# Kernel optimization log

Hardware: AMD Instinct MI355X
Metric: run time of the kernel (lower is better)

## Reference

```python
import jax, jax.numpy as jnp
import numpy as np

H = 256          # hidden_size
S = 4            # feature size (2D -> 4)
T_OUT = 16       # args.output // args.skip
HT_LIM = 100.0   # hardtanh limit
B = 16384
OBS = 16


def lstm_cell(x, h, c, Wih, Whh, bih, bhh):
    # PyTorch gate order: i, f, g, o
    g = x @ Wih.T + h @ Whh.T + bih + bhh  # [B, 4H]
    i, f, gg, o = jnp.split(g, 4, axis=-1)
    c = jax.nn.sigmoid(f) * c + jax.nn.sigmoid(i) * jnp.tanh(gg)
    h = jax.nn.sigmoid(o) * jnp.tanh(c)
    return h, c


def encode(seq, Wih, Whh, bih, bhh):
    # seq: [B, T, S]; single-layer LSTM, return final (h, c)
    h0 = jnp.zeros((seq.shape[0], H), seq.dtype)
    def step(carry, x):
        h, c = carry
        return lstm_cell(x, h, c, Wih, Whh, bih, bhh), None
    (h, c), _ = jax.lax.scan(step, (h0, h0), jnp.swapaxes(seq, 0, 1))
    return h, c


def setup_inputs() -> dict:
    key = jax.random.key(0)
    ks = jax.random.split(key, 32)
    sc = 0.05
    def W(k, shape):
        return (jax.random.normal(k, shape, jnp.float32) * sc)
    inp = {
        'speed': jax.random.normal(ks[0], (B, OBS, S), jnp.float32),
        'pos': jax.random.normal(ks[1], (B, OBS, S), jnp.float32),
        # speed encoder LSTM
        'sp_Wih': W(ks[2], (4 * H, S)), 'sp_Whh': W(ks[3], (4 * H, H)),
        'sp_bih': W(ks[4], (4 * H,)), 'sp_bhh': W(ks[5], (4 * H,)),
        # pos encoder LSTM
        'po_Wih': W(ks[6], (4 * H, S)), 'po_Whh': W(ks[7], (4 * H, H)),
        'po_bih': W(ks[8], (4 * H,)), 'po_bhh': W(ks[9], (4 * H,)),
        # speed decoder LSTMCell
        'dsp_Wih': W(ks[10], (4 * H, S)), 'dsp_Whh': W(ks[11], (4 * H, H)),
        'dsp_bih': W(ks[12], (4 * H,)), 'dsp_bhh': W(ks[13], (4 * H,)),
        # crossing decoder LSTMCell
        'dcr_Wih': W(ks[14], (4 * H, S)), 'dcr_Whh': W(ks[15], (4 * H, H)),
        'dcr_bih': W(ks[16], (4 * H,)), 'dcr_bhh': W(ks[17], (4 * H,)),
        # heads
        'fc_speed_W': W(ks[18], (S, H)), 'fc_speed_b': W(ks[19], (S,)),
        'fc_cross_W': W(ks[20], (2, H)), 'fc_cross_b': W(ks[21], (2,)),
        'emb_W': W(ks[22], (S, H)), 'emb_b': W(ks[23], (S,)),
    }
    return inp


def reference(speed, pos,
              sp_Wih, sp_Whh, sp_bih, sp_bhh,
              po_Wih, po_Whh, po_bih, po_bhh,
              dsp_Wih, dsp_Whh, dsp_bih, dsp_bhh,
              dcr_Wih, dcr_Whh, dcr_bih, dcr_bhh,
              fc_speed_W, fc_speed_b, fc_cross_W, fc_cross_b,
              emb_W, emb_b):
    hsp, csp = encode(speed, sp_Wih, sp_Whh, sp_bih, sp_bhh)
    hpo, cpo = encode(pos, po_Wih, po_Whh, po_bih, po_bhh)
    h0 = hpo + hsp
    c0 = cpo + csp

    # ---- speed decoder: feed back hardtanh(fc_speed(h)) (detached) ----
    def sp_step(carry, _):
        h, c, x = carry
        h, c = lstm_cell(x, h, c, dsp_Wih, dsp_Whh, dsp_bih, dsp_bhh)
        out = jnp.clip(h @ fc_speed_W.T + fc_speed_b, -HT_LIM, HT_LIM)
        return (h, c, jax.lax.stop_gradient(out)), out
    _, sp_outs = jax.lax.scan(sp_step, (h0, c0, speed[:, -1, :]), None, length=T_OUT)
    speed_outputs = jnp.swapaxes(sp_outs, 0, 1)  # [B, T_OUT, S]

    # ---- crossing decoder: feed back relu(pos_embedding(h)) (detached) ----
    def cr_step(carry, _):
        h, c, x = carry
        h, c = lstm_cell(x, h, c, dcr_Wih, dcr_Whh, dcr_bih, dcr_bhh)
        logits = jax.nn.relu(h @ fc_cross_W.T + fc_cross_b)  # [B, 2]
        out = jax.nn.softmax(logits, axis=1)
        x_next = jax.lax.stop_gradient(jax.nn.relu(h @ emb_W.T + emb_b))
        return (h, c, x_next), out
    _, cr_outs = jax.lax.scan(cr_step, (h0, c0, pos[:, -1, :]), None, length=T_OUT)
    crossing_outputs = jnp.swapaxes(cr_outs, 0, 1)  # [B, T_OUT, 2]

    return (speed_outputs, crossing_outputs)
```

## Files before the change

### kernel.cpp

```cpp
#include <hip/hip_runtime.h>

typedef unsigned short ushort_t;
typedef __bf16 bf16x8 __attribute__((ext_vector_type(8)));
typedef float f32x4 __attribute__((ext_vector_type(4)));

#define PACK_W_ELEMS (8*9*8*512)
#define HEAD_ELEMS   (9*512)
#define PACK_TOTAL   (4*PACK_W_ELEMS + 2*HEAD_ELEMS)
#define FLAG_OFS     PACK_TOTAL

__device__ __forceinline__ float bf2f(ushort_t u){ return __uint_as_float(((unsigned)u)<<16); }
__device__ __forceinline__ ushort_t f2bf(float f){
  __bf16 h = (__bf16)f;
  return *(ushort_t*)&h;
}
__device__ __forceinline__ float rcp_(float x){ return __builtin_amdgcn_rcpf(x); }

__device__ __forceinline__ int sniff_f32(const ushort_t* w){
  int f32 = 0;
  #pragma unroll
  for (int i = 0; i < 32; ++i){
    float f = bf2f(w[2*i]);
    if (!(f > -8.f && f < 8.f)) f32 = 1;
  }
  return f32;
}
__device__ __forceinline__ float ldin(const ushort_t* p, int i, int f32){
  return f32 ? ((const float*)p)[i] : bf2f(p[i]);
}
__device__ __forceinline__ ushort_t ldw(const ushort_t* p, int i, int f32){
  return f32 ? f2bf(((const float*)p)[i]) : p[i];
}

struct PackArgs {
  const ushort_t* wih[4]; const ushort_t* whh[4];
  const ushort_t* bih[4]; const ushort_t* bhh[4];
  const ushort_t* fcsp_w; const ushort_t* fcsp_b;
  const ushort_t* fccr_w; const ushort_t* fccr_b;
  const ushort_t* emb_w;  const ushort_t* emb_b;
  ushort_t* ws;
};

__global__ void pack_kernel(PackArgs a){
  const int f32 = sniff_f32(a.whh[0]);
  int idx = blockIdx.x*256 + threadIdx.x;
  if (blockIdx.x == 0 && threadIdx.x == 0) *(int*)(a.ws + FLAG_OFS) = f32;
  const int total_w = 4*PACK_W_ELEMS;
  if (idx < total_w){
    int l = idx / PACK_W_ELEMS;
    int r = idx % PACK_W_ELEMS;
    int j = r & 7;
    int lane = (r>>3) & 63;
    int tile = r >> 9;
    int gu = tile & 7;
    int kt = (tile >> 3) % 9;
    int wv = tile / 72;
    int g = gu >> 1, u = gu & 1;
    int n = (g*16 + wv*2 + u)*16 + (lane & 15);
    int k = kt*32 + ((lane>>4)<<3) + j;
    ushort_t v = 0;
    if (k < 256)       v = ldw(a.whh[l], n*256 + k, f32);
    else if (k < 260)  v = ldw(a.wih[l], n*4 + (k-256), f32);
    else if (k == 260) v = f2bf(ldin(a.bih[l], n, f32) + ldin(a.bhh[l], n, f32));
    a.ws[l*PACK_W_ELEMS + r] = v;
    return;
  }
  idx -= total_w;
  if (idx < 2*HEAD_ELEMS){
    int which = idx / HEAD_ELEMS;
    int r = idx % HEAD_ELEMS;
    int j = r & 7; int lane = (r>>3)&63; int kt = r>>9;
    int n = lane & 15; int k = kt*32 + ((lane>>4)<<3) + j;
    ushort_t v = 0;
    if (which == 0){
      if (n < 4){
        if (k < 256)       v = ldw(a.fcsp_w, n*256 + k, f32);
        else if (k == 260) v = f2bf(ldin(a.fcsp_b, n, f32));
      }
    } else {
      if (n < 4){
        if (k < 256)       v = ldw(a.emb_w, n*256 + k, f32);
        else if (k == 260) v = f2bf(ldin(a.emb_b, n, f32));
      } else if (n < 6){
        if (k < 256)       v = ldw(a.fccr_w, (n-4)*256 + k, f32);
        else if (k == 260) v = f2bf(ldin(a.fccr_b, n-4, f32));
      }
    }
    a.ws[total_w + idx] = v;
  }
}

#define PRE4(bw, s0, s1, s2, s3)                \
  bf16x8 s0 = *(const bf16x8*)&(bw)[0*512];     \
  bf16x8 s1 = *(const bf16x8*)&(bw)[1*512];     \
  bf16x8 s2 = *(const bf16x8*)&(bw)[2*512];     \
  bf16x8 s3 = *(const bf16x8*)&(bw)[3*512];

__device__ __forceinline__ void gate_gemm(const ushort_t* __restrict__ Aln,
                                          const ushort_t* __restrict__ bw,
                                          f32x4 (&acc)[4][8], int lane,
                                          bf16x8 p0, bf16x8 p1, bf16x8 p2, bf16x8 p3){
  #pragma unroll
  for (int i = 0; i < 4; ++i)
    #pragma unroll
    for (int j = 0; j < 8; ++j) acc[i][j] = (f32x4){0.f,0.f,0.f,0.f};
  const ushort_t* bp = bw;
  #pragma unroll 1
  for (int kt = 0; kt < 9; ++kt){
    bf16x8 q0 = *(const bf16x8*)&bp[4*512];
    bf16x8 q1 = *(const bf16x8*)&bp[5*512];
    bf16x8 q2 = *(const bf16x8*)&bp[6*512];
    bf16x8 q3 = *(const bf16x8*)&bp[7*512];
    bf16x8 a0 = *(const bf16x8*)&Aln[(0*9+kt)*512];
    bf16x8 a1 = *(const bf16x8*)&Aln[(1*9+kt)*512];
    bf16x8 a2 = *(const bf16x8*)&Aln[(2*9+kt)*512];
    bf16x8 a3 = *(const bf16x8*)&Aln[(3*9+kt)*512];
    acc[0][0] = __builtin_amdgcn_mfma_f32_16x16x32_bf16(a0, p0, acc[0][0], 0, 0, 0);
    acc[1][0] = __builtin_amdgcn_mfma_f32_16x16x32_bf16(a1, p0, acc[1][0], 0, 0, 0);
    acc[2][0] = __builtin_amdgcn_mfma_f32_16x16x32_bf16(a2, p0, acc[2][0], 0, 0, 0);
    acc[3][0] = __builtin_amdgcn_mfma_f32_16x16x32_bf16(a3, p0, acc[3][0], 0, 0, 0);
    acc[0][1] = __builtin_amdgcn_mfma_f32_16x16x32_bf16(a0, p1, acc[0][1], 0, 0, 0);
    acc[1][1] = __builtin_amdgcn_mfma_f32_16x16x32_bf16(a1, p1, acc[1][1], 0, 0, 0);
    acc[2][1] = __builtin_amdgcn_mfma_f32_16x16x32_bf16(a2, p1, acc[2][1], 0, 0, 0);
    acc[3][1] = __builtin_amdgcn_mfma_f32_16x16x32_bf16(a3, p1, acc[3][1], 0, 0, 0);
    acc[0][2] = __builtin_amdgcn_mfma_f32_16x16x32_bf16(a0, p2, acc[0][2], 0, 0, 0);
    acc[1][2] = __builtin_amdgcn_mfma_f32_16x16x32_bf16(a1, p2, acc[1][2], 0, 0, 0);
    acc[2][2] = __builtin_amdgcn_mfma_f32_16x16x32_bf16(a2, p2, acc[2][2], 0, 0, 0);
    acc[3][2] = __builtin_amdgcn_mfma_f32_16x16x32_bf16(a3, p2, acc[3][2], 0, 0, 0);
    acc[0][3] = __builtin_amdgcn_mfma_f32_16x16x32_bf16(a0, p3, acc[0][3], 0, 0, 0);
    acc[1][3] = __builtin_amdgcn_mfma_f32_16x16x32_bf16(a1, p3, acc[1][3], 0, 0, 0);
    acc[2][3] = __builtin_amdgcn_mfma_f32_16x16x32_bf16(a2, p3, acc[2][3], 0, 0, 0);
    acc[3][3] = __builtin_amdgcn_mfma_f32_16x16x32_bf16(a3, p3, acc[3][3], 0, 0, 0);
    if (kt < 8){
      p0 = *(const bf16x8*)&bp[4096 + 0*512];
      p1 = *(const bf16x8*)&bp[4096 + 1*512];
      p2 = *(const bf16x8*)&bp[4096 + 2*512];
      p3 = *(const bf16x8*)&bp[4096 + 3*512];
    }
    acc[0][4] = __builtin_amdgcn_mfma_f32_16x16x32_bf16(a0, q0, acc[0][4], 0, 0, 0);
    acc[1][4] = __builtin_amdgcn_mfma_f32_16x16x32_bf16(a1, q0, acc[1][4], 0, 0, 0);
    acc[2][4] = __builtin_amdgcn_mfma_f32_16x16x32_bf16(a2, q0, acc[2][4], 0, 0, 0);
    acc[3][4] = __builtin_amdgcn_mfma_f32_16x16x32_bf16(a3, q0, acc[3][4], 0, 0, 0);
    acc[0][5] = __builtin_amdgcn_mfma_f32_16x16x32_bf16(a0, q1, acc[0][5], 0, 0, 0);
    acc[1][5] = __builtin_amdgcn_mfma_f32_16x16x32_bf16(a1, q1, acc[1][5], 0, 0, 0);
    acc[2][5] = __builtin_amdgcn_mfma_f32_16x16x32_bf16(a2, q1, acc[2][5], 0, 0, 0);
    acc[3][5] = __builtin_amdgcn_mfma_f32_16x16x32_bf16(a3, q1, acc[3][5], 0, 0, 0);
    acc[0][6] = __builtin_amdgcn_mfma_f32_16x16x32_bf16(a0, q2, acc[0][6], 0, 0, 0);
    acc[1][6] = __builtin_amdgcn_mfma_f32_16x16x32_bf16(a1, q2, acc[1][6], 0, 0, 0);
    acc[2][6] = __builtin_amdgcn_mfma_f32_16x16x32_bf16(a2, q2, acc[2][6], 0, 0, 0);
    acc[3][6] = __builtin_amdgcn_mfma_f32_16x16x32_bf16(a3, q2, acc[3][6], 0, 0, 0);
    acc[0][7] = __builtin_amdgcn_mfma_f32_16x16x32_bf16(a0, q3, acc[0][7], 0, 0, 0);
    acc[1][7] = __builtin_amdgcn_mfma_f32_16x16x32_bf16(a1, q3, acc[1][7], 0, 0, 0);
    acc[2][7] = __builtin_amdgcn_mfma_f32_16x16x32_bf16(a2, q3, acc[2][7], 0, 0, 0);
    acc[3][7] = __builtin_amdgcn_mfma_f32_16x16x32_bf16(a3, q3, acc[3][7], 0, 0, 0);
    bp += 4096;
  }
}

__device__ __forceinline__ void gates_wb(f32x4 (&acc)[4][8], float (&cw)[4][2][4],
                                         ushort_t* __restrict__ Ap, int wbBase){
  #pragma unroll
  for (int mt = 0; mt < 4; ++mt)
    #pragma unroll
    for (int u = 0; u < 2; ++u)
      #pragma unroll
      for (int r = 0; r < 4; ++r){
        const float i_ = acc[mt][u][r];
        const float f_ = acc[mt][2+u][r];
        const float g_ = acc[mt][4+u][r];
        const float o_ = acc[mt][6+u][r];
        const float ei = __expf(-i_);
        const float ef = __expf(-f_);
        const float eg = __expf(-2.0f*g_);
        const float di = 1.0f + ei, df = 1.0f + ef;
        const float dg = 1.0f + eg, ng = 1.0f - eg;
        const float dig = di*dg;
        const float cn = (cw[mt][u][r]*dig + ng*df) * rcp_(df*dig);
        const float eo = __expf(-o_);
        const float ec = __expf(-2.0f*cn);
        const float hn = (1.0f - ec) * rcp_((1.0f + eo)*(1.0f + ec));
        cw[mt][u][r] = cn;
        Ap[mt*4608 + u*256 + r*8 + wbBase] = f2bf(hn);
      }
}

__global__ __launch_bounds__(512, 2) void pvlstm_main(
    const ushort_t* __restrict__ ws,
    const ushort_t* __restrict__ speed,
    const ushort_t* __restrict__ pos,
    void* __restrict__ outv)
{
  __shared__ ushort_t ApS[4*9*512];
  __shared__ ushort_t ApP[4*9*512];
  __shared__ ushort_t xsS[64*64];
  __shared__ ushort_t xsP[64*64];
  __shared__ float    ostS[64*64];
  __shared__ float    ostC[64*32];

  const int f32   = *(const int*)(ws + FLAG_OFS);
  const int tid   = threadIdx.x;
  const int lane  = tid & 63;
  const int w     = tid >> 6;
  const int col16 = lane & 15;
  const int quad  = lane >> 4;
  const int brow0 = blockIdx.x * 64;
  const int wbBase = w*512 + (col16>>3)*128 + quad*32 + (col16&7);

  ushort_t* outu = (ushort_t*)outv;
  float*    outf = (float*)outv;

  const ushort_t* headsp = ws + 4*PACK_W_ELEMS;
  const ushort_t* headcr = headsp + HEAD_ELEMS;
  const ushort_t* aS  = ApS + lane*8;
  const ushort_t* aP  = ApP + lane*8;
  const ushort_t* bwS  = ws + 0*PACK_W_ELEMS + (size_t)w*36864 + (size_t)lane*8;
  const ushort_t* bwP  = ws + 1*PACK_W_ELEMS + (size_t)w*36864 + (size_t)lane*8;
  const ushort_t* bwDS = ws + 2*PACK_W_ELEMS + (size_t)w*36864 + (size_t)lane*8;
  const ushort_t* bwDC = ws + 3*PACK_W_ELEMS + (size_t)w*36864 + (size_t)lane*8;

  float cwA[4][2][4], cwB[4][2][4];
  f32x4 acc[4][8];

  for (int i = tid; i < 4096; i += 512){
    int gi = (brow0 + (i>>6))*64 + (i&63);
    xsS[i] = f2bf(ldin(speed, gi, f32));
    xsP[i] = f2bf(ldin(pos,   gi, f32));
  }
  for (int i = tid; i < 4*9*512/2; i += 512){
    ((unsigned*)ApS)[i] = 0u; ((unsigned*)ApP)[i] = 0u;
  }
  #pragma unroll
  for (int mt = 0; mt < 4; ++mt)
    #pragma unroll
    for (int u = 0; u < 2; ++u)
      #pragma unroll
      for (int r = 0; r < 4; ++r){ cwA[mt][u][r] = 0.f; cwB[mt][u][r] = 0.f; }
  __syncthreads();
  if (tid < 64){
    ushort_t* xpS = &ApS[((tid>>4)*9 + 8)*512 + (tid&15)*8];
    ushort_t* xpP = &ApP[((tid>>4)*9 + 8)*512 + (tid&15)*8];
    *(uint2*)xpS = *(const uint2*)&xsS[tid*64];
    xpS[4] = (ushort_t)0x3f80;
    xpP[4] = (ushort_t)0x3f80;
  }
  __syncthreads();

  for (int t = 0; t < 16; ++t){
    {
      PRE4(bwS, s0, s1, s2, s3)
      if (t > 0) gates_wb(acc, cwB, ApP, wbBase);
      if (tid < 64)
        *(uint2*)&ApP[((tid>>4)*9 + 8)*512 + (tid&15)*8] = *(const uint2*)&xsP[tid*64 + t*4];
      gate_gemm(aS, bwS, acc, lane, s0, s1, s2, s3);
    }
    __syncthreads();
    {
      PRE4(bwP, s0, s1, s2, s3)
      gates_wb(acc, cwA, ApS, wbBase);
      if (t < 15 && tid < 64)
        *(uint2*)&ApS[((tid>>4)*9 + 8)*512 + (tid&15)*8] = *(const uint2*)&xsS[tid*64 + t*4 + 4];
      gate_gemm(aP, bwP, acc, lane, s0, s1, s2, s3);
    }
    __syncthreads();
  }
  #pragma unroll
  for (int mt = 0; mt < 4; ++mt)
    #pragma unroll
    for (int u = 0; u < 2; ++u)
      #pragma unroll
      for (int r = 0; r < 4; ++r){
        const float i_ = acc[mt][u][r];
        const float f_ = acc[mt][2+u][r];
        const float g_ = acc[mt][4+u][r];
        const float o_ = acc[mt][6+u][r];
        const float ei = __expf(-i_);
        const float ef = __expf(-f_);
        const float eg = __expf(-2.0f*g_);
        const float di = 1.0f + ei, df = 1.0f + ef;
        const float dg = 1.0f + eg, ng = 1.0f - eg;
        const float dig = di*dg;
        const float cn = (cwB[mt][u][r]*dig + ng*df) * rcp_(df*dig);
        const float eo = __expf(-o_);
        const float ec = __expf(-2.0f*cn);
        const float hn = (1.0f - ec) * rcp_((1.0f + eo)*(1.0f + ec));
        const float c0 = cwA[mt][u][r] + cn;
        cwA[mt][u][r] = c0; cwB[mt][u][r] = c0;
        const int ad = mt*4608 + u*256 + r*8 + wbBase;
        ushort_t h0 = f2bf(bf2f(ApS[ad]) + hn);
        ApS[ad] = h0; ApP[ad] = h0;
      }
  if (tid < 64){
    *(uint2*)&ApS[((tid>>4)*9 + 8)*512 + (tid&15)*8] = *(const uint2*)&xsS[tid*64 + 60];
    *(uint2*)&ApP[((tid>>4)*9 + 8)*512 + (tid&15)*8] = *(const uint2*)&xsP[tid*64 + 60];
  }
  __syncthreads();

  for (int t = 0; t < 16; ++t){
    {
      PRE4(bwDS, s0, s1, s2, s3)
      if (t > 0 && w >= 4){
        const int mt = w - 4;
        f32x4 hacc = (f32x4){0.f,0.f,0.f,0.f};
        #pragma unroll
        for (int kt = 0; kt < 9; ++kt){
          bf16x8 a  = *(const bf16x8*)&aP[(mt*9+kt)*512];
          bf16x8 bv = *(const bf16x8*)&headcr[((size_t)kt*64 + lane)*8];
          hacc = __builtin_amdgcn_mfma_f32_16x16x32_bf16(a, bv, hacc, 0, 0, 0);
        }
        const int s = col16;
        #pragma unroll
        for (int r = 0; r < 4; ++r){
          float v = fmaxf(hacc[r], 0.f);
          const float o = __shfl_xor(v, 1, 64);
          const int m = mt*16 + quad*4 + r;
          if (s < 4){
            ApP[(mt*9+8)*512 + (m&15)*8 + s] = f2bf(v);
          } else if (s < 6){
            const float mx = fmaxf(v, o);
            const float e0 = __expf(v-mx), e1 = __expf(o-mx);
            ostC[m*32 + (t-1)*2 + (s-4)] = e0*rcp_(e0+e1);
          }
        }
      }
      gate_gemm(aS, bwDS, acc, lane, s0, s1, s2, s3);
    }
    __syncthreads();
    {
      PRE4(bwDC, s0, s1, s2, s3)
      gates_wb(acc, cwA, ApS, wbBase);
      gate_gemm(aP, bwDC, acc, lane, s0, s1, s2, s3);
    }
    __syncthreads();
    gates_wb(acc, cwB, ApP, wbBase);
    if (w < 4){
      const int mt = w;
      f32x4 hacc = (f32x4){0.f,0.f,0.f,0.f};
      #pragma unroll
      for (int kt = 0; kt < 9; ++kt){
        bf16x8 a  = *(const bf16x8*)&aS[(mt*9+kt)*512];
        bf16x8 bv = *(const bf16x8*)&headsp[((size_t)kt*64 + lane)*8];
        hacc = __builtin_amdgcn_mfma_f32_16x16x32_bf16(a, bv, hacc, 0, 0, 0);
      }
      const int s = col16;
      if (s < 4){
        #pragma unroll
        for (int r = 0; r < 4; ++r){
          float v = fminf(fmaxf(hacc[r], -100.f), 100.f);
          const int m = mt*16 + quad*4 + r;
          ostS[m*64 + t*4 + s] = v;
          ApS[(mt*9+8)*512 + (m&15)*8 + s] = f2bf(v);
        }
      }
    }
    __syncthreads();
  }
  if (w >= 4){
    const int mt = w - 4;
    f32x4 hacc = (f32x4){0.f,0.f,0.f,0.f};
    #pragma unroll
    for (int kt = 0; kt < 9; ++kt){
      bf16x8 a  = *(const bf16x8*)&aP[(mt*9+kt)*512];
      bf16x8 bv = *(const bf16x8*)&headcr[((size_t)kt*64 + lane)*8];
      hacc = __builtin_amdgcn_mfma_f32_16x16x32_bf16(a, bv, hacc, 0, 0, 0);
    }
    const int s = col16;
    if (s >= 4 && s < 6){
      #pragma unroll
      for (int r = 0; r < 4; ++r){
        float v = fmaxf(hacc[r], 0.f);
        const float o = __shfl_xor(v, 1, 64);
        const int m = mt*16 + quad*4 + r;
        const float mx = fmaxf(v, o);
        const float e0 = __expf(v-mx), e1 = __expf(o-mx);
        ostC[m*32 + 15*2 + (s-4)] = e0*rcp_(e0+e1);
      }
    }
  }
  __syncthreads();

  for (int i = tid; i < 4096; i += 512){
    const int oi = (brow0 + (i>>6))*64 + (i&63);
    const float v = ostS[i];
    if (f32) outf[oi] = v; else outu[oi] = f2bf(v);
  }
  for (int i = tid; i < 2048; i += 512){
    const int oi = 1048576 + (brow0 + (i>>5))*32 + (i&31);
    const float v = ostC[i];
    if (f32) outf[oi] = v; else outu[oi] = f2bf(v);
  }
}

extern "C" void kernel_launch(void* const* d_in, const int* in_sizes, int n_in,
                              void* d_out, int out_size, void* d_ws, size_t ws_size,
                              hipStream_t stream) {
  PackArgs pa;
  pa.wih[0]=(const ushort_t*)d_in[2];  pa.whh[0]=(const ushort_t*)d_in[3];
  pa.bih[0]=(const ushort_t*)d_in[4];  pa.bhh[0]=(const ushort_t*)d_in[5];
  pa.wih[1]=(const ushort_t*)d_in[6];  pa.whh[1]=(const ushort_t*)d_in[7];
  pa.bih[1]=(const ushort_t*)d_in[8];  pa.bhh[1]=(const ushort_t*)d_in[9];
  pa.wih[2]=(const ushort_t*)d_in[10]; pa.whh[2]=(const ushort_t*)d_in[11];
  pa.bih[2]=(const ushort_t*)d_in[12]; pa.bhh[2]=(const ushort_t*)d_in[13];
  pa.wih[3]=(const ushort_t*)d_in[14]; pa.whh[3]=(const ushort_t*)d_in[15];
  pa.bih[3]=(const ushort_t*)d_in[16]; pa.bhh[3]=(const ushort_t*)d_in[17];
  pa.fcsp_w=(const ushort_t*)d_in[18]; pa.fcsp_b=(const ushort_t*)d_in[19];
  pa.fccr_w=(const ushort_t*)d_in[20]; pa.fccr_b=(const ushort_t*)d_in[21];
  pa.emb_w =(const ushort_t*)d_in[22]; pa.emb_b =(const ushort_t*)d_in[23];
  pa.ws = (ushort_t*)d_ws;

  hipLaunchKernelGGL(pack_kernel, dim3((PACK_TOTAL + 255)/256), dim3(256), 0, stream, pa);
  hipLaunchKernelGGL(pvlstm_main, dim3(256), dim3(512), 0, stream,
      (const ushort_t*)d_ws,
      (const ushort_t*)d_in[0], (const ushort_t*)d_in[1],
      d_out);
}
```

Baseline: 827.7 us.

## Stream gate weights through LDS with async global_load_lds double buffering

Gate weight tiles are now fetched with global_load_lds into a per-wave LDS buffer, issued one k-step ahead and chained across gate GEMMs, so the next weight block is in flight while the current MFMAs run. LDS reads use inline ds_read_b128 with explicit vmcnt/lgkmcnt waits and sched barriers, and __syncthreads is replaced by a raw barrier macro. The output staging arrays are dropped and results are written straight to global memory, which frees LDS for the weight buffers. This trades compiler scheduling freedom and more LDS traffic for hidden global-load latency, with risk from the hand-written wait counts.

```diff
diff --git a/kernel.cpp b/kernel.cpp
--- a/kernel.cpp
+++ b/kernel.cpp
@@ -3,6 +3,7 @@
 typedef unsigned short ushort_t;
 typedef __bf16 bf16x8 __attribute__((ext_vector_type(8)));
 typedef float f32x4 __attribute__((ext_vector_type(4)));
+typedef int i32x4_t __attribute__((ext_vector_type(4)));
 
 #define PACK_W_ELEMS (8*9*8*512)
 #define HEAD_ELEMS   (9*512)
@@ -90,70 +91,113 @@
   }
 }
 
-#define PRE4(bw, s0, s1, s2, s3)                \
-  bf16x8 s0 = *(const bf16x8*)&(bw)[0*512];     \
-  bf16x8 s1 = *(const bf16x8*)&(bw)[1*512];     \
-  bf16x8 s2 = *(const bf16x8*)&(bw)[2*512];     \
-  bf16x8 s3 = *(const bf16x8*)&(bw)[3*512];
-
-__device__ __forceinline__ void gate_gemm(const ushort_t* __restrict__ Aln,
-                                          const ushort_t* __restrict__ bw,
-                                          f32x4 (&acc)[4][8], int lane,
-                                          bf16x8 p0, bf16x8 p1, bf16x8 p2, bf16x8 p3){
+#define BAR() do { asm volatile("s_waitcnt lgkmcnt(0)" ::: "memory"); \
+                   __builtin_amdgcn_s_barrier();                      \
+                   asm volatile("" ::: "memory"); } while(0)
+#define WAITV4() do { asm volatile("s_waitcnt vmcnt(4)"); __builtin_amdgcn_sched_barrier(0); } while(0)
+#define WAITV0() do { asm volatile("s_waitcnt vmcnt(0)"); __builtin_amdgcn_sched_barrier(0); } while(0)
+#define WAITL0() do { asm volatile("s_waitcnt lgkmcnt(0)"); __builtin_amdgcn_sched_barrier(0); } while(0)
+
+__device__ __forceinline__ unsigned lds_off(const void* p){
+  return (unsigned)(size_t)(const __attribute__((address_space(3))) void*)p;
+}
+__device__ __forceinline__ bf16x8 dsr16(unsigned off){
+  i32x4_t v;
+  asm volatile("ds_read_b128 %0, %1" : "=v"(v) : "v"(off));
+  return *(bf16x8*)&v;
+}
+__device__ __forceinline__ void issue4(const ushort_t* gsrc, ushort_t* ldst){
+  #pragma unroll
+  for (int i = 0; i < 4; ++i)
+    __builtin_amdgcn_global_load_lds(
+      (const __attribute__((address_space(1))) void*)(gsrc + i*512),
+      (__attribute__((address_space(3))) void*)(ldst + i*512), 16, 0, 0);
+}
+
+#define MFMA16(H, B0, B1, B2, B3)                                                      \
+  acc[0][H+0] = __builtin_amdgcn_mfma_f32_16x16x32_bf16(a0, B0, acc[0][H+0], 0,0,0);   \
+  acc[1][H+0] = __builtin_amdgcn_mfma_f32_16x16x32_bf16(a1, B0, acc[1][H+0], 0,0,0);   \
+  acc[2][H+0] = __builtin_amdgcn_mfma_f32_16x16x32_bf16(a2, B0, acc[2][H+0], 0,0,0);   \
+  acc[3][H+0] = __builtin_amdgcn_mfma_f32_16x16x32_bf16(a3, B0, acc[3][H+0], 0,0,0);   \
+  acc[0][H+1] = __builtin_amdgcn_mfma_f32_16x16x32_bf16(a0, B1, acc[0][H+1], 0,0,0);   \
+  acc[1][H+1] = __builtin_amdgcn_mfma_f32_16x16x32_bf16(a1, B1, acc[1][H+1], 0,0,0);   \
+  acc[2][H+1] = __builtin_amdgcn_mfma_f32_16x16x32_bf16(a2, B1, acc[2][H+1], 0,0,0);   \
+  acc[3][H+1] = __builtin_amdgcn_mfma_f32_16x16x32_bf16(a3, B1, acc[3][H+1], 0,0,0);   \
+  acc[0][H+2] = __builtin_amdgcn_mfma_f32_16x16x32_bf16(a0, B2, acc[0][H+2], 0,0,0);   \
+  acc[1][H+2] = __builtin_amdgcn_mfma_f32_16x16x32_bf16(a1, B2, acc[1][H+2], 0,0,0);   \
+  acc[2][H+2] = __builtin_amdgcn_mfma_f32_16x16x32_bf16(a2, B2, acc[2][H+2], 0,0,0);   \
+  acc[3][H+2] = __builtin_amdgcn_mfma_f32_16x16x32_bf16(a3, B2, acc[3][H+2], 0,0,0);   \
+  acc[0][H+3] = __builtin_amdgcn_mfma_f32_16x16x32_bf16(a0, B3, acc[0][H+3], 0,0,0);   \
+  acc[1][H+3] = __builtin_amdgcn_mfma_f32_16x16x32_bf16(a1, B3, acc[1][H+3], 0,0,0);   \
+  acc[2][H+3] = __builtin_amdgcn_mfma_f32_16x16x32_bf16(a2, B3, acc[2][H+3], 0,0,0);   \
+  acc[3][H+3] = __builtin_amdgcn_mfma_f32_16x16x32_bf16(a3, B3, acc[3][H+3], 0,0,0);
+
+__device__ __forceinline__ void gate_gemm(
+    unsigned aOff,
+    unsigned bOff,
+    const ushort_t* __restrict__ bwCur,
+    const ushort_t* __restrict__ bwNext,
+    ushort_t* blsW,
+    int hasNext,
+    f32x4 (&acc)[4][8])
+{
   #pragma unroll
   for (int i = 0; i < 4; ++i)
     #pragma unroll
     for (int j = 0; j < 8; ++j) acc[i][j] = (f32x4){0.f,0.f,0.f,0.f};
-  const ushort_t* bp = bw;
+  bf16x8 a0, a1, a2, a3;
+  const ushort_t* pIss = bwCur + 4096;
   #pragma unroll 1
-  for (int kt = 0; kt < 9; ++kt){
-    bf16x8 q0 = *(const bf16x8*)&bp[4*512];
-    bf16x8 q1 = *(const bf16x8*)&bp[5*512];
-    bf16x8 q2 = *(const bf16x8*)&bp[6*512];
-    bf16x8 q3 = *(const bf16x8*)&bp[7*512];
-    bf16x8 a0 = *(const bf16x8*)&Aln[(0*9+kt)*512];
-    bf16x8 a1 = *(const bf16x8*)&Aln[(1*9+kt)*512];
-    bf16x8 a2 = *(const bf16x8*)&Aln[(2*9+kt)*512];
-    bf16x8 a3 = *(const bf16x8*)&Aln[(3*9+kt)*512];
-    acc[0][0] = __builtin_amdgcn_mfma_f32_16x16x32_bf16(a0, p0, acc[0][0], 0, 0, 0);
-    acc[1][0] = __builtin_amdgcn_mfma_f32_16x16x32_bf16(a1, p0, acc[1][0], 0, 0, 0);
-    acc[2][0] = __builtin_amdgcn_mfma_f32_16x16x32_bf16(a2, p0, acc[2][0], 0, 0, 0);
-    acc[3][0] = __builtin_amdgcn_mfma_f32_16x16x32_bf16(a3, p0, acc[3][0], 0, 0, 0);
-    acc[0][1] = __builtin_amdgcn_mfma_f32_16x16x32_bf16(a0, p1, acc[0][1], 0, 0, 0);
-    acc[1][1] = __builtin_amdgcn_mfma_f32_16x16x32_bf16(a1, p1, acc[1][1], 0, 0, 0);
-    acc[2][1] = __builtin_amdgcn_mfma_f32_16x16x32_bf16(a2, p1, acc[2][1], 0, 0, 0);
-    acc[3][1] = __builtin_amdgcn_mfma_f32_16x16x32_bf16(a3, p1, acc[3][1], 0, 0, 0);
-    acc[0][2] = __builtin_amdgcn_mfma_f32_16x16x32_bf16(a0, p2, acc[0][2], 0, 0, 0);
-    acc[1][2] = __builtin_amdgcn_mfma_f32_16x16x32_bf16(a1, p2, acc[1][2], 0, 0, 0);
-    acc[2][2] = __builtin_amdgcn_mfma_f32_16x16x32_bf16(a2, p2, acc[2][2], 0, 0, 0);
-    acc[3][2] = __builtin_amdgcn_mfma_f32_16x16x32_bf16(a3, p2, acc[3][2], 0, 0, 0);
-    acc[0][3] = __builtin_amdgcn_mfma_f32_16x16x32_bf16(a0, p3, acc[0][3], 0, 0, 0);
-    acc[1][3] = __builtin_amdgcn_mfma_f32_16x16x32_bf16(a1, p3, acc[1][3], 0, 0, 0);
-    acc[2][3] = __builtin_amdgcn_mfma_f32_16x16x32_bf16(a2, p3, acc[2][3], 0, 0, 0);
-    acc[3][3] = __builtin_amdgcn_mfma_f32_16x16x32_bf16(a3, p3, acc[3][3], 0, 0, 0);
-    if (kt < 8){
-      p0 = *(const bf16x8*)&bp[4096 + 0*512];
-      p1 = *(const bf16x8*)&bp[4096 + 1*512];
-      p2 = *(const bf16x8*)&bp[4096 + 2*512];
-      p3 = *(const bf16x8*)&bp[4096 + 3*512];
-    }
-    acc[0][4] = __builtin_amdgcn_mfma_f32_16x16x32_bf16(a0, q0, acc[0][4], 0, 0, 0);
-    acc[1][4] = __builtin_amdgcn_mfma_f32_16x16x32_bf16(a1, q0, acc[1][4], 0, 0, 0);
-    acc[2][4] = __builtin_amdgcn_mfma_f32_16x16x32_bf16(a2, q0, acc[2][4], 0, 0, 0);
-    acc[3][4] = __builtin_amdgcn_mfma_f32_16x16x32_bf16(a3, q0, acc[3][4], 0, 0, 0);
-    acc[0][5] = __builtin_amdgcn_mfma_f32_16x16x32_bf16(a0, q1, acc[0][5], 0, 0, 0);
-    acc[1][5] = __builtin_amdgcn_mfma_f32_16x16x32_bf16(a1, q1, acc[1][5], 0, 0, 0);
-    acc[2][5] = __builtin_amdgcn_mfma_f32_16x16x32_bf16(a2, q1, acc[2][5], 0, 0, 0);
-    acc[3][5] = __builtin_amdgcn_mfma_f32_16x16x32_bf16(a3, q1, acc[3][5], 0, 0, 0);
-    acc[0][6] = __builtin_amdgcn_mfma_f32_16x16x32_bf16(a0, q2, acc[0][6], 0, 0, 0);
-    acc[1][6] = __builtin_amdgcn_mfma_f32_16x16x32_bf16(a1, q2, acc[1][6], 0, 0, 0);
-    acc[2][6] = __builtin_amdgcn_mfma_f32_16x16x32_bf16(a2, q2, acc[2][6], 0, 0, 0);
-    acc[3][6] = __builtin_amdgcn_mfma_f32_16x16x32_bf16(a3, q2, acc[3][6], 0, 0, 0);
-    acc[0][7] = __builtin_amdgcn_mfma_f32_16x16x32_bf16(a0, q3, acc[0][7], 0, 0, 0);
-    acc[1][7] = __builtin_amdgcn_mfma_f32_16x16x32_bf16(a1, q3, acc[1][7], 0, 0, 0);
-    acc[2][7] = __builtin_amdgcn_mfma_f32_16x16x32_bf16(a2, q3, acc[2][7], 0, 0, 0);
-    acc[3][7] = __builtin_amdgcn_mfma_f32_16x16x32_bf16(a3, q3, acc[3][7], 0, 0, 0);
-    bp += 4096;
+  for (int kt = 0; kt < 8; ++kt){
+    WAITV4();
+    bf16x8 b0 = dsr16(bOff + 0);
+    bf16x8 b1 = dsr16(bOff + 1024);
+    bf16x8 b2 = dsr16(bOff + 2048);
+    bf16x8 b3 = dsr16(bOff + 3072);
+    {
+      const unsigned aK = aOff + (unsigned)kt*1024u;
+      a0 = dsr16(aK);
+      a1 = dsr16(aK + 9216);
+      a2 = dsr16(aK + 18432);
+      a3 = dsr16(aK + 27648);
+    }
+    WAITL0();
+    issue4(pIss, blsW);
+    MFMA16(0, b0, b1, b2, b3)
+    WAITV4();
+    bf16x8 c0 = dsr16(bOff + 32768);
+    bf16x8 c1 = dsr16(bOff + 32768 + 1024);
+    bf16x8 c2 = dsr16(bOff + 32768 + 2048);
+    bf16x8 c3 = dsr16(bOff + 32768 + 3072);
+    WAITL0();
+    issue4(pIss + 2048, blsW + 16384);
+    MFMA16(4, c0, c1, c2, c3)
+    pIss += 4096;
+  }
+  {
+    WAITV4();
+    bf16x8 b0 = dsr16(bOff + 0);
+    bf16x8 b1 = dsr16(bOff + 1024);
+    bf16x8 b2 = dsr16(bOff + 2048);
+    bf16x8 b3 = dsr16(bOff + 3072);
+    {
+      const unsigned aK = aOff + 8u*1024u;
+      a0 = dsr16(aK);
+      a1 = dsr16(aK + 9216);
+      a2 = dsr16(aK + 18432);
+      a3 = dsr16(aK + 27648);
+    }
+    WAITL0();
+    if (hasNext) issue4(bwNext, blsW);
+    MFMA16(0, b0, b1, b2, b3)
+    if (hasNext) { WAITV4(); } else { WAITV0(); }
+    bf16x8 c0 = dsr16(bOff + 32768);
+    bf16x8 c1 = dsr16(bOff + 32768 + 1024);
+    bf16x8 c2 = dsr16(bOff + 32768 + 2048);
+    bf16x8 c3 = dsr16(bOff + 32768 + 3072);
+    WAITL0();
+    if (hasNext) issue4(bwNext + 2048, blsW + 16384);
+    MFMA16(4, c0, c1, c2, c3)
   }
 }
 
@@ -194,8 +238,7 @@
   __shared__ ushort_t ApP[4*9*512];
   __shared__ ushort_t xsS[64*64];
   __shared__ ushort_t xsP[64*64];
-  __shared__ float    ostS[64*64];
-  __shared__ float    ostC[64*32];
+  __shared__ ushort_t Bls[2][8][2048];
 
   const int f32   = *(const int*)(ws + FLAG_OFS);
   const int tid   = threadIdx.x;
@@ -218,6 +261,11 @@
   const ushort_t* bwDS = ws + 2*PACK_W_ELEMS + (size_t)w*36864 + (size_t)lane*8;
   const ushort_t* bwDC = ws + 3*PACK_W_ELEMS + (size_t)w*36864 + (size_t)lane*8;
 
+  ushort_t* blsW = &Bls[0][w][0];
+  const unsigned bOff  = lds_off(blsW) + (unsigned)lane*16u;
+  const unsigned aOffS = lds_off(ApS) + (unsigned)lane*16u;
+  const unsigned aOffP = lds_off(ApP) + (unsigned)lane*16u;
+
   float cwA[4][2][4], cwB[4][2][4];
   f32x4 acc[4][8];
 
@@ -235,7 +283,7 @@
     for (int u = 0; u < 2; ++u)
       #pragma unroll
       for (int r = 0; r < 4; ++r){ cwA[mt][u][r] = 0.f; cwB[mt][u][r] = 0.f; }
-  __syncthreads();
+  BAR();
   if (tid < 64){
     ushort_t* xpS = &ApS[((tid>>4)*9 + 8)*512 + (tid&15)*8];
     ushort_t* xpP = &ApP[((tid>>4)*9 + 8)*512 + (tid&15)*8];
@@ -243,25 +291,21 @@
     xpS[4] = (ushort_t)0x3f80;
     xpP[4] = (ushort_t)0x3f80;
   }
-  __syncthreads();
+  BAR();
+  issue4(bwS,        blsW);
+  issue4(bwS + 2048, blsW + 16384);
 
   for (int t = 0; t < 16; ++t){
-    {
-      PRE4(bwS, s0, s1, s2, s3)
-      if (t > 0) gates_wb(acc, cwB, ApP, wbBase);
-      if (tid < 64)
-        *(uint2*)&ApP[((tid>>4)*9 + 8)*512 + (tid&15)*8] = *(const uint2*)&xsP[tid*64 + t*4];
-      gate_gemm(aS, bwS, acc, lane, s0, s1, s2, s3);
-    }
-    __syncthreads();
-    {
-      PRE4(bwP, s0, s1, s2, s3)
-      gates_wb(acc, cwA, ApS, wbBase);
-      if (t < 15 && tid < 64)
-        *(uint2*)&ApS[((tid>>4)*9 + 8)*512 + (tid&15)*8] = *(const uint2*)&xsS[tid*64 + t*4 + 4];
-      gate_gemm(aP, bwP, acc, lane, s0, s1, s2, s3);
-    }
-    __syncthreads();
+    if (t > 0) gates_wb(acc, cwB, ApP, wbBase);
+    if (tid < 64)
+      *(uint2*)&ApP[((tid>>4)*9 + 8)*512 + (tid&15)*8] = *(const uint2*)&xsP[tid*64 + t*4];
+    gate_gemm(aOffS, bOff, bwS, bwP, blsW, 1, acc);
+    BAR();
+    gates_wb(acc, cwA, ApS, wbBase);
+    if (t < 15 && tid < 64)
+      *(uint2*)&ApS[((tid>>4)*9 + 8)*512 + (tid&15)*8] = *(const uint2*)&xsS[tid*64 + t*4 + 4];
+    gate_gemm(aOffP, bOff, bwP, (t < 15) ? bwS : bwDS, blsW, 1, acc);
+    BAR();
   }
   #pragma unroll
   for (int mt = 0; mt < 4; ++mt)
@@ -293,44 +337,40 @@
     *(uint2*)&ApS[((tid>>4)*9 + 8)*512 + (tid&15)*8] = *(const uint2*)&xsS[tid*64 + 60];
     *(uint2*)&ApP[((tid>>4)*9 + 8)*512 + (tid&15)*8] = *(const uint2*)&xsP[tid*64 + 60];
   }
-  __syncthreads();
+  BAR();
 
   for (int t = 0; t < 16; ++t){
-    {
-      PRE4(bwDS, s0, s1, s2, s3)
-      if (t > 0 && w >= 4){
-        const int mt = w - 4;
-        f32x4 hacc = (f32x4){0.f,0.f,0.f,0.f};
-        #pragma unroll
-        for (int kt = 0; kt < 9; ++kt){
-          bf16x8 a  = *(const bf16x8*)&aP[(mt*9+kt)*512];
-          bf16x8 bv = *(const bf16x8*)&headcr[((size_t)kt*64 + lane)*8];
-          hacc = __builtin_amdgcn_mfma_f32_16x16x32_bf16(a, bv, hacc, 0, 0, 0);
+    if (t > 0 && w >= 4){
+      const int mt = w - 4;
+      f32x4 hacc = (f32x4){0.f,0.f,0.f,0.f};
+      #pragma unroll
+      for (int kt = 0; kt < 9; ++kt){
+        bf16x8 a  = *(const bf16x8*)&aP[(mt*9+kt)*512];
+        bf16x8 bv = *(const bf16x8*)&headcr[((size_t)kt*64 + lane)*8];
+        hacc = __builtin_amdgcn_mfma_f32_16x16x32_bf16(a, bv, hacc, 0, 0, 0);
+      }
+      const int s = col16;
+      #pragma unroll
+      for (int r = 0; r < 4; ++r){
+        float v = fmaxf(hacc[r], 0.f);
+        const float o = __shfl_xor(v, 1, 64);
+        const int m = mt*16 + quad*4 + r;
+        if (s < 4){
+          ApP[(mt*9+8)*512 + (m&15)*8 + s] = f2bf(v);
+        } else if (s < 6){
+          const float mx = fmaxf(v, o);
+          const float e0 = __expf(v-mx), e1 = __expf(o-mx);
+          const float pv = e0*rcp_(e0+e1);
+          const int oi = 1048576 + (brow0 + m)*32 + (t-1)*2 + (s-4);
+          if (f32) outf[oi] = pv; else outu[oi] = f2bf(pv);
         }
-        const int s = col16;
-        #pragma unroll
-        for (int r = 0; r < 4; ++r){
-          float v = fmaxf(hacc[r], 0.f);
-          const float o = __shfl_xor(v, 1, 64);
-          const int m = mt*16 + quad*4 + r;
-          if (s < 4){
-            ApP[(mt*9+8)*512 + (m&15)*8 + s] = f2bf(v);
-          } else if (s < 6){
-            const float mx = fmaxf(v, o);
-            const float e0 = __expf(v-mx), e1 = __expf(o-mx);
-            ostC[m*32 + (t-1)*2 + (s-4)] = e0*rcp_(e0+e1);
-          }
-        }
-      }
-      gate_gemm(aS, bwDS, acc, lane, s0, s1, s2, s3);
-    }
-    __syncthreads();
-    {
-      PRE4(bwDC, s0, s1, s2, s3)
-      gates_wb(acc, cwA, ApS, wbBase);
-      gate_gemm(aP, bwDC, acc, lane, s0, s1, s2, s3);
-    }
-    __syncthreads();
+      }
+    }
+    gate_gemm(aOffS, bOff, bwDS, bwDC, blsW, 1, acc);
+    BAR();
+    gates_wb(acc, cwA, ApS, wbBase);
+    gate_gemm(aOffP, bOff, bwDC, bwDS, blsW, (t < 15) ? 1 : 0, acc);
+    BAR();
     gates_wb(acc, cwB, ApP, wbBase);
     if (w < 4){
       const int mt = w;
@@ -347,12 +387,13 @@
         for (int r = 0; r < 4; ++r){
           float v = fminf(fmaxf(hacc[r], -100.f), 100.f);
           const int m = mt*16 + quad*4 + r;
-          ostS[m*64 + t*4 + s] = v;
+          const int oi = (brow0 + m)*64 + t*4 + s;
+          if (f32) outf[oi] = v; else outu[oi] = f2bf(v);
           ApS[(mt*9+8)*512 + (m&15)*8 + s] = f2bf(v);
         }
       }
     }
-    __syncthreads();
+    BAR();
   }
   if (w >= 4){
     const int mt = w - 4;
@@ -372,21 +413,11 @@
         const int m = mt*16 + quad*4 + r;
         const float mx = fmaxf(v, o);
         const float e0 = __expf(v-mx), e1 = __expf(o-mx);
-        ostC[m*32 + 15*2 + (s-4)] = e0*rcp_(e0+e1);
-      }
-    }
-  }
-  __syncthreads();
-
-  for (int i = tid; i < 4096; i += 512){
-    const int oi = (brow0 + (i>>6))*64 + (i&63);
-    const float v = ostS[i];
-    if (f32) outf[oi] = v; else outu[oi] = f2bf(v);
-  }
-  for (int i = tid; i < 2048; i += 512){
-    const int oi = 1048576 + (brow0 + (i>>5))*32 + (i&31);
-    const float v = ostC[i];
-    if (f32) outf[oi] = v; else outu[oi] = f2bf(v);
+        const float pv = e0*rcp_(e0+e1);
+        const int oi = 1048576 + (brow0 + m)*32 + 15*2 + (s-4);
+        if (f32) outf[oi] = pv; else outu[oi] = f2bf(pv);
+      }
+    }
   }
 }
 
```

After: 910.2 us. +10.0%, slower.
